# Kernel tuning notes

Hardware: AMD Instinct MI355X
Metric: run time of the kernel (lower is better)

## Reference

```python
import jax, jax.numpy as jnp
import numpy as np

N, E, D_IN, D_H, D_OUT = 8000, 256000, 128, 128, 64
TEMP = 10.0       # config temperature.value (non-learnable)
WEIGHT = 1.0      # config weight.value (non-learnable)
LN_EPS = 1e-5


def _gcn_conv(x, W, b, src, dst, n):
    # PyG GCNConv: add self loops, sym-normalized aggregation, then bias.
    h = x @ W
    loop = jnp.arange(n)
    s = jnp.concatenate([src, loop])
    d = jnp.concatenate([dst, loop])
    deg = jnp.zeros((n,), h.dtype).at[d].add(1.0)
    dinv = jax.lax.rsqrt(jnp.maximum(deg, 1e-12))
    norm = dinv[s] * dinv[d]                       # [E+N]
    out = jax.ops.segment_sum(h[s] * norm[:, None], d, num_segments=n)
    return out + b


def _entropy_gradient(x, A, temperature, normalize):
    # E_i = 0.5 * sum_j A_ij ||x_i - x_j||^2  (dense adjacency, as in repo)
    sq = jnp.sum(x * x, axis=1)                    # [N]
    Ax = A @ x                                     # [N,d]
    deg = A.sum(axis=1)                            # [N]
    En = 0.5 * (deg * sq + A @ sq - 2.0 * jnp.sum(x * Ax, axis=1))
    if normalize:
        En = En / (jnp.max(En) + 1e-12)
    logits = -En / temperature
    P = jax.nn.softmax(logits)
    logP = jax.nn.log_softmax(logits)
    S = -jnp.sum(P * logP)
    c = P * (logP + S) / temperature               # dS/dE_k
    # dS/dx_i = c_i*(deg_i x_i - (Ax)_i) + (A^T c)_i x_i - (A^T (c*x))_i
    ATc = A.T @ c
    return (c[:, None] * (deg[:, None] * x - Ax)
            + ATc[:, None] * x - A.T @ (c[:, None] * x))


def _layer_norm(x, gamma, beta):
    mu = jnp.mean(x, axis=-1, keepdims=True)
    var = jnp.mean(jnp.square(x - mu), axis=-1, keepdims=True)
    return (x - mu) * jax.lax.rsqrt(var + LN_EPS) * gamma + beta


def setup_inputs() -> dict:
    key = jax.random.key(0)
    ks = jax.random.split(key, 6)
    def w(k, i, o):
        return jax.random.normal(k, (i, o), jnp.float32) / np.sqrt(i).astype(np.float32)
    return {
        "x": jax.random.normal(ks[0], (N, D_IN), jnp.float32),
        "edge_index": jax.random.randint(ks[1], (2, E), 0, N),
        "W1": w(ks[2], D_IN, D_H), "b1": jnp.zeros((D_H,), jnp.float32),
        "W2": w(ks[3], D_H, D_H), "b2": jnp.zeros((D_H,), jnp.float32),
        "W_out": w(ks[4], D_H, D_OUT), "b_out": jnp.zeros((D_OUT,), jnp.float32),
        "ln_gamma": jnp.ones((D_H,), jnp.float32),
        "ln_beta": jnp.zeros((D_H,), jnp.float32),
    }


def reference(x, edge_index, W1, b1, W2, b2, W_out, b_out, ln_gamma, ln_beta):
    n = x.shape[0]
    src, dst = edge_index[0], edge_index[1]
    # dense adjacency (to_dense_adj sums duplicate edges)
    A = jnp.zeros((n, n), x.dtype).at[src, dst].add(1.0)
    for W, b in ((W1, b1), (W2, b2)):
        h = _gcn_conv(x, W, b, src, dst, n)
        eg = jax.lax.stop_gradient(_entropy_gradient(h, A, TEMP, True))
        h = h + WEIGHT * eg
        h = jax.nn.relu(h)
        x = _layer_norm(h, ln_gamma, ln_beta)
    embedding = _gcn_conv(x, W_out, b_out, src, dst, n)
    return embedding
```

## Files before the change

### kernel.cpp

```cpp
#include <hip/hip_runtime.h>
#include <hip/hip_bf16.h>

#define DH 128
#define NCOPY 8

static constexpr float TEMP_ = 10.0f;
static constexpr float LN_EPS_ = 1e-5f;

__device__ __forceinline__ unsigned short f2bf(float f) {
  union { float f; unsigned int i; } v; v.f = f;
  unsigned int b = v.i + 0x7FFFu + ((v.i >> 16) & 1u);
  return (unsigned short)(b >> 16);
}
__device__ __forceinline__ void dec2(unsigned int u, float& lo, float& hi) {
  union { unsigned int i; float f; } a, b;
  a.i = u << 16; b.i = u & 0xFFFF0000u;
  lo = a.f; hi = b.f;
}
__device__ __forceinline__ void dec8(uint4 u, float* o) {
  dec2(u.x, o[0], o[1]); dec2(u.y, o[2], o[3]);
  dec2(u.z, o[4], o[5]); dec2(u.w, o[6], o[7]);
}
__device__ __forceinline__ unsigned int pack2(float lo, float hi) {
  return (unsigned int)f2bf(lo) | ((unsigned int)f2bf(hi) << 16);
}

__device__ __forceinline__ float grp_sum16(float v) {
  #pragma unroll
  for (int o = 8; o > 0; o >>= 1) v += __shfl_down(v, o, 16);
  return __shfl(v, 0, 16);
}

__device__ __forceinline__ float blkred(float v, bool mx, float* s4) {
  const int t = threadIdx.x;
  #pragma unroll
  for (int o = 32; o > 0; o >>= 1) {
    float u = __shfl_down(v, o, 64);
    v = mx ? fmaxf(v, u) : v + u;
  }
  __syncthreads();
  if ((t & 63) == 0) s4[t >> 6] = v;
  __syncthreads();
  float r = mx ? fmaxf(fmaxf(s4[0], s4[1]), fmaxf(s4[2], s4[3]))
               : (s4[0] + s4[1]) + (s4[2] + s4[3]);
  __syncthreads();
  return r;
}

__global__ __launch_bounds__(256) void k_gemm1_hist(const float* __restrict__ X,
                                                    const float* __restrict__ W,
                                                    unsigned short* __restrict__ Hb,
                                                    const int* __restrict__ ei, int E,
                                                    int* cnt_d, int* cnt_s,
                                                    int NT, int N) {
  __shared__ float Ws[64 * DH];
  __shared__ float xs[16 * 128];
  const int t = threadIdx.x;
  if ((int)blockIdx.x < NT) {
    const int row0 = blockIdx.x * 16;
    const float4* xg = (const float4*)(X + row0 * 128);
    float4* xs4 = (float4*)xs;
    xs4[t] = xg[t];
    xs4[t + 256] = xg[t + 256];
    const int c = t & 127, rg = t >> 7;
    float acc[8];
    #pragma unroll
    for (int r = 0; r < 8; ++r) acc[r] = 0.f;
    for (int kt = 0; kt < 2; ++kt) {
      __syncthreads();
      for (int i = t; i < 64 * DH; i += 256) Ws[i] = W[kt * 64 * DH + i];
      __syncthreads();
      for (int k = 0; k < 64; ++k) {
        float wv = Ws[k * DH + c];
        #pragma unroll
        for (int r = 0; r < 8; ++r)
          acc[r] += xs[(rg * 8 + r) * 128 + kt * 64 + k] * wv;
      }
    }
    #pragma unroll
    for (int r = 0; r < 8; ++r)
      Hb[(row0 + rg * 8 + r) * DH + c] = f2bf(acc[r]);
  } else {
    const int nb = gridDim.x - NT;
    for (int e = (blockIdx.x - NT) * 256 + t; e < E; e += nb * 256) {
      int cp = (e >> 5) & (NCOPY - 1);
      atomicAdd(&cnt_s[cp * N + ei[e]], 1);
      atomicAdd(&cnt_d[cp * N + ei[E + e]], 1);
    }
  }
}

template <int DOUT>
__global__ __launch_bounds__(256) void k_gemm(const float* __restrict__ X,
                                              const float* __restrict__ W,
                                              unsigned short* __restrict__ Hb) {
  __shared__ float Ws[64 * DOUT];
  __shared__ float xs[16 * 128];
  const int t = threadIdx.x;
  const int row0 = blockIdx.x * 16;

  const float4* xg = (const float4*)(X + row0 * 128);
  float4* xs4 = (float4*)xs;
  xs4[t] = xg[t];
  xs4[t + 256] = xg[t + 256];

  constexpr int RPT = (16 * DOUT) / 256;
  const int c = t % DOUT;
  const int rg = t / DOUT;
  float acc[RPT];
  #pragma unroll
  for (int r = 0; r < RPT; ++r) acc[r] = 0.f;

  for (int kt = 0; kt < 2; ++kt) {
    __syncthreads();
    for (int i = t; i < 64 * DOUT; i += 256) Ws[i] = W[kt * 64 * DOUT + i];
    __syncthreads();
    for (int k = 0; k < 64; ++k) {
      float wv = Ws[k * DOUT + c];
      #pragma unroll
      for (int r = 0; r < RPT; ++r)
        acc[r] += xs[(rg * RPT + r) * 128 + kt * 64 + k] * wv;
    }
  }
  #pragma unroll
  for (int r = 0; r < RPT; ++r)
    Hb[(row0 + rg * RPT + r) * DOUT + c] = f2bf(acc[r]);
}

__global__ __launch_bounds__(256) void k_scan_a(int* cnt_d, int* cnt_s,
                                                int* off_d, int* off_s,
                                                int* bsum,
                                                float* dinv, float* dego, int n) {
  __shared__ int ws4[4];
  const int t = threadIdx.x;
  const int dir = blockIdx.x >> 5, blk = blockIdx.x & 31;
  int* cnt = dir ? cnt_s : cnt_d;
  int* off = dir ? off_s : off_d;
  const int NPB = (n + 31) >> 5;
  const int i = blk * NPB + t;
  const bool valid = (t < NPB) && (i < n);
  int tot = 0;
  if (valid) {
    #pragma unroll
    for (int c = 0; c < NCOPY; ++c) tot += cnt[c * n + i];
  }
  const int lane = t & 63, w = t >> 6;
  int v = tot;
  #pragma unroll
  for (int o = 1; o < 64; o <<= 1) {
    int u = __shfl_up(v, o, 64);
    if (lane >= o) v += u;
  }
  if (lane == 63) ws4[w] = v;
  __syncthreads();
  int wbase = 0;
  #pragma unroll
  for (int k = 0; k < 4; ++k) wbase += (k < w) ? ws4[k] : 0;
  const int excl = wbase + v - tot;
  if (valid) {
    off[i] = excl;
    if (dir == 0) dinv[i] = rsqrtf((float)tot + 1.0f);
    else          dego[i] = (float)tot;
  }
  if (t == 0) {
    int bt = 0;
    #pragma unroll
    for (int k = 0; k < 4; ++k) bt += ws4[k];
    bsum[dir * 32 + blk] = bt;
  }
}

__global__ __launch_bounds__(256) void k_scan_b(int* cnt_d, int* cnt_s,
                                                int* off_d, int* off_s,
                                                int* base_d, int* base_s,
                                                const int* __restrict__ bsum, int n) {
  __shared__ int sb;
  const int t = threadIdx.x;
  const int dir = blockIdx.x >> 5, blk = blockIdx.x & 31;
  int* cnt  = dir ? cnt_s  : cnt_d;
  int* off  = dir ? off_s  : off_d;
  int* base = dir ? base_s : base_d;
  if (t == 0) {
    int s = 0;
    for (int k = 0; k < blk; ++k) s += bsum[dir * 32 + k];
    sb = s;
  }
  __syncthreads();
  const int bbase = sb;
  const int NPB = (n + 31) >> 5;
  const int i = blk * NPB + t;
  if (t < NPB && i < n) {
    int o = bbase + off[i];
    off[i] = o;
    int rc = o;
    #pragma unroll
    for (int c = 0; c < NCOPY; ++c) {
      base[c * n + i] = rc;
      rc += cnt[c * n + i];
      cnt[c * n + i] = 0;
    }
  }
  if (t == 1 && blk == 31) {
    int s = 0;
    for (int k = 0; k < 32; ++k) s += bsum[dir * 32 + k];
    off[n] = s;
  }
}

__global__ void k_fill(const int* __restrict__ ei, int E,
                       const int* __restrict__ base_d, const int* __restrict__ base_s,
                       int* cnt_d, int* cnt_s, int* idx_d, int* idx_s, int N) {
  int e = blockIdx.x * blockDim.x + threadIdx.x;
  if (e < E) {
    int cp = (e >> 5) & (NCOPY - 1);
    int s = ei[e], d = ei[E + e];
    int p = atomicAdd(&cnt_d[cp * N + d], 1);
    idx_d[base_d[cp * N + d] + p] = s;
    int q = atomicAdd(&cnt_s[cp * N + s], 1);
    idx_s[base_s[cp * N + s] + q] = d;
  }
}

__global__ __launch_bounds__(256) void k_conv_agg(const unsigned short* __restrict__ Hb,
                                                  const float* __restrict__ dinv,
                                                  const float* __restrict__ b,
                                                  const int* __restrict__ off_d,
                                                  const int* __restrict__ idx_d,
                                                  float* __restrict__ G,
                                                  unsigned short* __restrict__ Gb,
                                                  float* __restrict__ sq) {
  const int lane = threadIdx.x & 15;
  const int i = blockIdx.x * 16 + (threadIdx.x >> 4);
  const uint4* Hv = (const uint4*)Hb;
  const float di = dinv[i];
  float acc[8];
  {
    float t8[8]; dec8(Hv[i * 16 + lane], t8);
    #pragma unroll
    for (int k = 0; k < 8; ++k) acc[k] = di * t8[k];
  }
  int o = off_d[i];
  const int oe = off_d[i + 1];
  for (; o + 8 <= oe; o += 8) {
    int s[8]; float dv[8]; uint4 r[8];
    #pragma unroll
    for (int j = 0; j < 8; ++j) s[j] = idx_d[o + j];
    #pragma unroll
    for (int j = 0; j < 8; ++j) { r[j] = Hv[s[j] * 16 + lane]; dv[j] = dinv[s[j]]; }
    #pragma unroll
    for (int j = 0; j < 8; ++j) {
      float t8[8]; dec8(r[j], t8);
      #pragma unroll
      for (int k = 0; k < 8; ++k) acc[k] = fmaf(dv[j], t8[k], acc[k]);
    }
  }
  for (; o < oe; ++o) {
    int s = idx_d[o];
    float dvs = dinv[s];
    float t8[8]; dec8(Hv[s * 16 + lane], t8);
    #pragma unroll
    for (int k = 0; k < 8; ++k) acc[k] = fmaf(dvs, t8[k], acc[k]);
  }
  const float4 b0 = ((const float4*)b)[lane * 2];
  const float4 b1 = ((const float4*)b)[lane * 2 + 1];
  float gi[8];
  gi[0] = fmaf(di, acc[0], b0.x); gi[1] = fmaf(di, acc[1], b0.y);
  gi[2] = fmaf(di, acc[2], b0.z); gi[3] = fmaf(di, acc[3], b0.w);
  gi[4] = fmaf(di, acc[4], b1.x); gi[5] = fmaf(di, acc[5], b1.y);
  gi[6] = fmaf(di, acc[6], b1.z); gi[7] = fmaf(di, acc[7], b1.w);
  ((float4*)G)[i * 32 + lane * 2]     = make_float4(gi[0], gi[1], gi[2], gi[3]);
  ((float4*)G)[i * 32 + lane * 2 + 1] = make_float4(gi[4], gi[5], gi[6], gi[7]);
  uint4 gp;
  gp.x = pack2(gi[0], gi[1]); gp.y = pack2(gi[2], gi[3]);
  gp.z = pack2(gi[4], gi[5]); gp.w = pack2(gi[6], gi[7]);
  ((uint4*)Gb)[i * 16 + lane] = gp;
  float s2 = 0.f;
  #pragma unroll
  for (int k = 0; k < 8; ++k) s2 += gi[k] * gi[k];
  s2 = grp_sum16(s2);
  if (lane == 0) sq[i] = s2;
}

__global__ __launch_bounds__(256) void k_ax_en(const float* __restrict__ G,
                                               const unsigned short* __restrict__ Gb,
                                               const float* __restrict__ sq,
                                               const float* __restrict__ dego,
                                               const int* __restrict__ off_s,
                                               const int* __restrict__ idx_s,
                                               float* __restrict__ Ax,
                                               float* __restrict__ En) {
  const int lane = threadIdx.x & 15;
  const int i = blockIdx.x * 16 + (threadIdx.x >> 4);
  const uint4* Gv = (const uint4*)Gb;
  float axf[8];
  #pragma unroll
  for (int k = 0; k < 8; ++k) axf[k] = 0.f;
  float asq = 0.f;
  int o = off_s[i];
  const int oe = off_s[i + 1];
  for (; o + 8 <= oe; o += 8) {
    int s[8]; float qv[8]; uint4 r[8];
    #pragma unroll
    for (int j = 0; j < 8; ++j) s[j] = idx_s[o + j];
    #pragma unroll
    for (int j = 0; j < 8; ++j) { r[j] = Gv[s[j] * 16 + lane]; qv[j] = sq[s[j]]; }
    #pragma unroll
    for (int j = 0; j < 8; ++j) {
      float t8[8]; dec8(r[j], t8);
      asq += qv[j];
      #pragma unroll
      for (int k = 0; k < 8; ++k) axf[k] += t8[k];
    }
  }
  for (; o < oe; ++o) {
    int s = idx_s[o];
    float t8[8]; dec8(Gv[s * 16 + lane], t8);
    asq += sq[s];
    #pragma unroll
    for (int k = 0; k < 8; ++k) axf[k] += t8[k];
  }
  ((float4*)Ax)[i * 32 + lane * 2]     = make_float4(axf[0], axf[1], axf[2], axf[3]);
  ((float4*)Ax)[i * 32 + lane * 2 + 1] = make_float4(axf[4], axf[5], axf[6], axf[7]);
  const float4 g0 = ((const float4*)G)[i * 32 + lane * 2];
  const float4 g1 = ((const float4*)G)[i * 32 + lane * 2 + 1];
  float dot = g0.x * axf[0] + g0.y * axf[1] + g0.z * axf[2] + g0.w * axf[3]
            + g1.x * axf[4] + g1.y * axf[5] + g1.z * axf[6] + g1.w * axf[7];
  dot = grp_sum16(dot);
  if (lane == 0) En[i] = 0.5f * (dego[i] * sq[i] + asq - 2.f * dot);
}

__global__ __launch_bounds__(256) void k_combine_ln(const float* __restrict__ G,
                                                    const unsigned short* __restrict__ Gb,
                                                    const float* __restrict__ Ax,
                                                    const float* __restrict__ En,
                                                    const float* __restrict__ dego,
                                                    const int* __restrict__ off_d,
                                                    const int* __restrict__ idx_d,
                                                    const float* __restrict__ gamma,
                                                    const float* __restrict__ beta,
                                                    float* __restrict__ Xout, int n) {
  __shared__ float s4[4];
  const int t = threadIdx.x;
  float mloc = -3.0e38f;
  for (int k = t; k < n; k += 256) mloc = fmaxf(mloc, En[k]);
  const float m = blkred(mloc, true, s4);
  const float invden = -1.0f / ((m + 1e-12f) * TEMP_);
  float se = 0.f, sl = 0.f;
  for (int k = t; k < n; k += 256) {
    float li = En[k] * invden;
    float e = __expf(li);
    se += e; sl += e * li;
  }
  se = blkred(se, false, s4);
  sl = blkred(sl, false, s4);
  const float logZ = __logf(se);
  const float S = logZ - sl / se;
  const float cmul = (1.0f / se) * (1.0f / TEMP_);
  const float cadd = S - logZ;

  const int lane = t & 15;
  const int i = blockIdx.x * 16 + (t >> 4);
  const uint4* Gv = (const uint4*)Gb;
  const float4 g0 = ((const float4*)G)[i * 32 + lane * 2];
  const float4 g1 = ((const float4*)G)[i * 32 + lane * 2 + 1];
  const float gi[8] = { g0.x, g0.y, g0.z, g0.w, g1.x, g1.y, g1.z, g1.w };
  float tf[8];
  #pragma unroll
  for (int k = 0; k < 8; ++k) tf[k] = 0.f;
  float atc = 0.f;
  int o = off_d[i];
  const int oe = off_d[i + 1];
  for (; o + 8 <= oe; o += 8) {
    int s[8]; float ev[8]; uint4 r[8];
    #pragma unroll
    for (int j = 0; j < 8; ++j) s[j] = idx_d[o + j];
    #pragma unroll
    for (int j = 0; j < 8; ++j) { r[j] = Gv[s[j] * 16 + lane]; ev[j] = En[s[j]]; }
    #pragma unroll
    for (int j = 0; j < 8; ++j) {
      float ls = ev[j] * invden;
      float cs = __expf(ls) * cmul * (ls + cadd);
      atc += cs;
      float t8[8]; dec8(r[j], t8);
      #pragma unroll
      for (int k = 0; k < 8; ++k) tf[k] = fmaf(cs, t8[k], tf[k]);
    }
  }
  for (; o < oe; ++o) {
    int s = idx_d[o];
    float ls = En[s] * invden;
    float cs = __expf(ls) * cmul * (ls + cadd);
    atc += cs;
    float t8[8]; dec8(Gv[s * 16 + lane], t8);
    #pragma unroll
    for (int k = 0; k < 8; ++k) tf[k] = fmaf(cs, t8[k], tf[k]);
  }
  const float li_i = En[i] * invden;
  const float ci = __expf(li_i) * cmul * (li_i + cadd);
  const float dg = dego[i];
  const float4 a0 = ((const float4*)Ax)[i * 32 + lane * 2];
  const float4 a1 = ((const float4*)Ax)[i * 32 + lane * 2 + 1];
  const float axi[8] = { a0.x, a0.y, a0.z, a0.w, a1.x, a1.y, a1.z, a1.w };
  float v[8];
  float ssum = 0.f;
  #pragma unroll
  for (int k = 0; k < 8; ++k) {
    v[k] = fmaxf(gi[k] + ci * (dg * gi[k] - axi[k]) + atc * gi[k] - tf[k], 0.f);
    ssum += v[k];
  }
  float mu = grp_sum16(ssum) * (1.f / 128.f);
  float vsum = 0.f;
  #pragma unroll
  for (int k = 0; k < 8; ++k) {
    v[k] -= mu;
    vsum += v[k] * v[k];
  }
  float var = grp_sum16(vsum) * (1.f / 128.f);
  float rs = rsqrtf(var + LN_EPS_);
  const float4 ga0 = ((const float4*)gamma)[lane * 2];
  const float4 ga1 = ((const float4*)gamma)[lane * 2 + 1];
  const float4 be0 = ((const float4*)beta)[lane * 2];
  const float4 be1 = ((const float4*)beta)[lane * 2 + 1];
  float4 o0, o1;
  o0.x = fmaf(v[0] * rs, ga0.x, be0.x); o0.y = fmaf(v[1] * rs, ga0.y, be0.y);
  o0.z = fmaf(v[2] * rs, ga0.z, be0.z); o0.w = fmaf(v[3] * rs, ga0.w, be0.w);
  o1.x = fmaf(v[4] * rs, ga1.x, be1.x); o1.y = fmaf(v[5] * rs, ga1.y, be1.y);
  o1.z = fmaf(v[6] * rs, ga1.z, be1.z); o1.w = fmaf(v[7] * rs, ga1.w, be1.w);
  ((float4*)Xout)[i * 32 + lane * 2]     = o0;
  ((float4*)Xout)[i * 32 + lane * 2 + 1] = o1;
}

__global__ __launch_bounds__(256) void k_final_agg(const unsigned short* __restrict__ Hb,
                                                   const float* __restrict__ dinv,
                                                   const float* __restrict__ bout,
                                                   const int* __restrict__ off_d,
                                                   const int* __restrict__ idx_d,
                                                   float* __restrict__ out) {
  const int lane = threadIdx.x & 7;
  const int i = blockIdx.x * 32 + (threadIdx.x >> 3);
  const uint4* Hv = (const uint4*)Hb;
  const float di = dinv[i];
  float acc[8];
  {
    float t8[8]; dec8(Hv[i * 8 + lane], t8);
    #pragma unroll
    for (int k = 0; k < 8; ++k) acc[k] = di * t8[k];
  }
  int o = off_d[i];
  const int oe = off_d[i + 1];
  for (; o + 8 <= oe; o += 8) {
    int s[8]; float dv[8]; uint4 r[8];
    #pragma unroll
    for (int j = 0; j < 8; ++j) s[j] = idx_d[o + j];
    #pragma unroll
    for (int j = 0; j < 8; ++j) { r[j] = Hv[s[j] * 8 + lane]; dv[j] = dinv[s[j]]; }
    #pragma unroll
    for (int j = 0; j < 8; ++j) {
      float t8[8]; dec8(r[j], t8);
      #pragma unroll
      for (int k = 0; k < 8; ++k) acc[k] = fmaf(dv[j], t8[k], acc[k]);
    }
  }
  for (; o < oe; ++o) {
    int s = idx_d[o];
    float dvs = dinv[s];
    float t8[8]; dec8(Hv[s * 8 + lane], t8);
    #pragma unroll
    for (int k = 0; k < 8; ++k) acc[k] = fmaf(dvs, t8[k], acc[k]);
  }
  const float4 b0 = ((const float4*)bout)[lane * 2];
  const float4 b1 = ((const float4*)bout)[lane * 2 + 1];
  float4 r0, r1;
  r0.x = fmaf(di, acc[0], b0.x); r0.y = fmaf(di, acc[1], b0.y);
  r0.z = fmaf(di, acc[2], b0.z); r0.w = fmaf(di, acc[3], b0.w);
  r1.x = fmaf(di, acc[4], b1.x); r1.y = fmaf(di, acc[5], b1.y);
  r1.z = fmaf(di, acc[6], b1.z); r1.w = fmaf(di, acc[7], b1.w);
  ((float4*)out)[i * 16 + lane * 2]     = r0;
  ((float4*)out)[i * 16 + lane * 2 + 1] = r1;
}

extern "C" void kernel_launch(void* const* d_in, const int* in_sizes, int n_in,
                              void* d_out, int out_size, void* d_ws, size_t ws_size,
                              hipStream_t stream) {
  const float* x    = (const float*)d_in[0];
  const int*   ei   = (const int*)d_in[1];
  const float* W1   = (const float*)d_in[2];
  const float* b1   = (const float*)d_in[3];
  const float* W2   = (const float*)d_in[4];
  const float* b2   = (const float*)d_in[5];
  const float* Wout = (const float*)d_in[6];
  const float* bout = (const float*)d_in[7];
  const float* gam  = (const float*)d_in[8];
  const float* bet  = (const float*)d_in[9];
  float* out = (float*)d_out;

  const int N = in_sizes[0] / DH;
  const int E = in_sizes[1] / 2;

  float* ws = (float*)d_ws;
  float* xf = ws;   ws += N * DH;
  float* G  = ws;   ws += N * DH;
  float* Ax = ws;   ws += N * DH;
  float* sq = ws;   ws += N;
  float* En = ws;   ws += N;
  float* dinv = ws; ws += N;
  float* dego = ws; ws += N;
  unsigned short* Hb = (unsigned short*)ws; ws += N * DH / 2;
  unsigned short* Gb = (unsigned short*)ws; ws += N * DH / 2;
  int* cnt_d  = (int*)ws; ws += NCOPY * N;
  int* cnt_s  = (int*)ws; ws += NCOPY * N;
  int* base_d = (int*)ws; ws += NCOPY * N;
  int* base_s = (int*)ws; ws += NCOPY * N;
  int* off_d  = (int*)ws; ws += N + 4;
  int* off_s  = (int*)ws; ws += N + 4;
  int* bsum   = (int*)ws; ws += 64;
  int* idx_d  = (int*)ws; ws += E;
  int* idx_s  = (int*)ws; ws += E;

  const int NT = N / 16;

  hipMemsetAsync(cnt_d, 0, 2 * NCOPY * N * sizeof(int), stream);
  k_gemm1_hist<<<NT + 256, 256, 0, stream>>>(x, W1, Hb, ei, E, cnt_d, cnt_s, NT, N);
  k_scan_a<<<64, 256, 0, stream>>>(cnt_d, cnt_s, off_d, off_s, bsum, dinv, dego, N);
  k_scan_b<<<64, 256, 0, stream>>>(cnt_d, cnt_s, off_d, off_s, base_d, base_s,
                                   bsum, N);
  k_fill<<<(E + 255) / 256, 256, 0, stream>>>(ei, E, base_d, base_s,
                                              cnt_d, cnt_s, idx_d, idx_s, N);

  for (int l = 0; l < 2; ++l) {
    if (l) k_gemm<DH><<<N / 16, 256, 0, stream>>>(xf, W2, Hb);
    k_conv_agg<<<N / 16, 256, 0, stream>>>(Hb, dinv, l ? b2 : b1, off_d, idx_d,
                                           G, Gb, sq);
    k_ax_en<<<N / 16, 256, 0, stream>>>(G, Gb, sq, dego, off_s, idx_s, Ax, En);
    k_combine_ln<<<N / 16, 256, 0, stream>>>(G, Gb, Ax, En, dego, off_d, idx_d,
                                             gam, bet, xf, N);
  }
  k_gemm<64><<<N / 16, 256, 0, stream>>>(xf, Wout, Hb);
  k_final_agg<<<N / 32, 256, 0, stream>>>(Hb, dinv, bout, off_d, idx_d, out);
}
```

Measured before the change: 249.2 us.

## Fuse LayerNorm with next GEMM and drop replicated histogram counters

Merges the combine+LayerNorm kernel with the following dense GEMM, so each block writes its normalized 16-row tile to shared memory and multiplies it by W2 or W_out directly. This removes the fp32 xf round trip through global memory and two kernel launches. Separately, the 8-way replicated degree counters used for the CSR histogram and fill are collapsed to a single copy, which simplifies the scans and drops the base arrays. That risks more atomic contention on hot nodes during the histogram and fill.

```diff
diff --git a/kernel.cpp b/kernel.cpp
--- a/kernel.cpp
+++ b/kernel.cpp
@@ -2,7 +2,6 @@
 #include <hip/hip_bf16.h>
 
 #define DH 128
-#define NCOPY 8
 
 static constexpr float TEMP_ = 10.0f;
 static constexpr float LN_EPS_ = 1e-5f;
@@ -51,8 +50,7 @@
                                                     const float* __restrict__ W,
                                                     unsigned short* __restrict__ Hb,
                                                     const int* __restrict__ ei, int E,
-                                                    int* cnt_d, int* cnt_s,
-                                                    int NT, int N) {
+                                                    int* cnt_d, int* cnt_s, int NT) {
   __shared__ float Ws[64 * DH];
   __shared__ float xs[16 * 128];
   const int t = threadIdx.x;
@@ -83,67 +81,25 @@
   } else {
     const int nb = gridDim.x - NT;
     for (int e = (blockIdx.x - NT) * 256 + t; e < E; e += nb * 256) {
-      int cp = (e >> 5) & (NCOPY - 1);
-      atomicAdd(&cnt_s[cp * N + ei[e]], 1);
-      atomicAdd(&cnt_d[cp * N + ei[E + e]], 1);
-    }
-  }
-}
-
-template <int DOUT>
-__global__ __launch_bounds__(256) void k_gemm(const float* __restrict__ X,
-                                              const float* __restrict__ W,
-                                              unsigned short* __restrict__ Hb) {
-  __shared__ float Ws[64 * DOUT];
-  __shared__ float xs[16 * 128];
-  const int t = threadIdx.x;
-  const int row0 = blockIdx.x * 16;
-
-  const float4* xg = (const float4*)(X + row0 * 128);
-  float4* xs4 = (float4*)xs;
-  xs4[t] = xg[t];
-  xs4[t + 256] = xg[t + 256];
-
-  constexpr int RPT = (16 * DOUT) / 256;
-  const int c = t % DOUT;
-  const int rg = t / DOUT;
-  float acc[RPT];
-  #pragma unroll
-  for (int r = 0; r < RPT; ++r) acc[r] = 0.f;
-
-  for (int kt = 0; kt < 2; ++kt) {
-    __syncthreads();
-    for (int i = t; i < 64 * DOUT; i += 256) Ws[i] = W[kt * 64 * DOUT + i];
-    __syncthreads();
-    for (int k = 0; k < 64; ++k) {
-      float wv = Ws[k * DOUT + c];
-      #pragma unroll
-      for (int r = 0; r < RPT; ++r)
-        acc[r] += xs[(rg * RPT + r) * 128 + kt * 64 + k] * wv;
-    }
-  }
-  #pragma unroll
-  for (int r = 0; r < RPT; ++r)
-    Hb[(row0 + rg * RPT + r) * DOUT + c] = f2bf(acc[r]);
-}
-
-__global__ __launch_bounds__(256) void k_scan_a(int* cnt_d, int* cnt_s,
-                                                int* off_d, int* off_s,
-                                                int* bsum,
+      atomicAdd(&cnt_s[ei[e]], 1);
+      atomicAdd(&cnt_d[ei[E + e]], 1);
+    }
+  }
+}
+
+__global__ __launch_bounds__(256) void k_scan_a(const int* __restrict__ cnt_d,
+                                                const int* __restrict__ cnt_s,
+                                                int* off_d, int* off_s, int* bsum,
                                                 float* dinv, float* dego, int n) {
   __shared__ int ws4[4];
   const int t = threadIdx.x;
   const int dir = blockIdx.x >> 5, blk = blockIdx.x & 31;
-  int* cnt = dir ? cnt_s : cnt_d;
+  const int* cnt = dir ? cnt_s : cnt_d;
   int* off = dir ? off_s : off_d;
   const int NPB = (n + 31) >> 5;
   const int i = blk * NPB + t;
   const bool valid = (t < NPB) && (i < n);
-  int tot = 0;
-  if (valid) {
-    #pragma unroll
-    for (int c = 0; c < NCOPY; ++c) tot += cnt[c * n + i];
-  }
+  int tot = valid ? cnt[i] : 0;
   const int lane = t & 63, w = t >> 6;
   int v = tot;
   #pragma unroll
@@ -172,14 +128,12 @@
 
 __global__ __launch_bounds__(256) void k_scan_b(int* cnt_d, int* cnt_s,
                                                 int* off_d, int* off_s,
-                                                int* base_d, int* base_s,
                                                 const int* __restrict__ bsum, int n) {
   __shared__ int sb;
   const int t = threadIdx.x;
   const int dir = blockIdx.x >> 5, blk = blockIdx.x & 31;
-  int* cnt  = dir ? cnt_s  : cnt_d;
-  int* off  = dir ? off_s  : off_d;
-  int* base = dir ? base_s : base_d;
+  int* cnt = dir ? cnt_s : cnt_d;
+  int* off = dir ? off_s : off_d;
   if (t == 0) {
     int s = 0;
     for (int k = 0; k < blk; ++k) s += bsum[dir * 32 + k];
@@ -190,15 +144,8 @@
   const int NPB = (n + 31) >> 5;
   const int i = blk * NPB + t;
   if (t < NPB && i < n) {
-    int o = bbase + off[i];
-    off[i] = o;
-    int rc = o;
-    #pragma unroll
-    for (int c = 0; c < NCOPY; ++c) {
-      base[c * n + i] = rc;
-      rc += cnt[c * n + i];
-      cnt[c * n + i] = 0;
-    }
+    off[i] = bbase + off[i];
+    cnt[i] = 0;
   }
   if (t == 1 && blk == 31) {
     int s = 0;
@@ -208,16 +155,15 @@
 }
 
 __global__ void k_fill(const int* __restrict__ ei, int E,
-                       const int* __restrict__ base_d, const int* __restrict__ base_s,
-                       int* cnt_d, int* cnt_s, int* idx_d, int* idx_s, int N) {
+                       const int* __restrict__ off_d, const int* __restrict__ off_s,
+                       int* cnt_d, int* cnt_s, int* idx_d, int* idx_s) {
   int e = blockIdx.x * blockDim.x + threadIdx.x;
   if (e < E) {
-    int cp = (e >> 5) & (NCOPY - 1);
     int s = ei[e], d = ei[E + e];
-    int p = atomicAdd(&cnt_d[cp * N + d], 1);
-    idx_d[base_d[cp * N + d] + p] = s;
-    int q = atomicAdd(&cnt_s[cp * N + s], 1);
-    idx_s[base_s[cp * N + s] + q] = d;
+    int p = atomicAdd(&cnt_d[d], 1);
+    idx_d[off_d[d] + p] = s;
+    int q = atomicAdd(&cnt_s[s], 1);
+    idx_s[off_s[s] + q] = d;
   }
 }
 
@@ -329,16 +275,21 @@
   if (lane == 0) En[i] = 0.5f * (dego[i] * sq[i] + asq - 2.f * dot);
 }
 
-__global__ __launch_bounds__(256) void k_combine_ln(const float* __restrict__ G,
-                                                    const unsigned short* __restrict__ Gb,
-                                                    const float* __restrict__ Ax,
-                                                    const float* __restrict__ En,
-                                                    const float* __restrict__ dego,
-                                                    const int* __restrict__ off_d,
-                                                    const int* __restrict__ idx_d,
-                                                    const float* __restrict__ gamma,
-                                                    const float* __restrict__ beta,
-                                                    float* __restrict__ Xout, int n) {
+template <int DOUT>
+__global__ __launch_bounds__(256) void k_combine_gemm(const float* __restrict__ G,
+                                                      const unsigned short* __restrict__ Gb,
+                                                      const float* __restrict__ Ax,
+                                                      const float* __restrict__ En,
+                                                      const float* __restrict__ dego,
+                                                      const int* __restrict__ off_d,
+                                                      const int* __restrict__ idx_d,
+                                                      const float* __restrict__ gamma,
+                                                      const float* __restrict__ beta,
+                                                      const float* __restrict__ W,
+                                                      unsigned short* __restrict__ Hb,
+                                                      int n) {
+  __shared__ float Ws[64 * DOUT];
+  __shared__ float xs[16 * 128];
   __shared__ float s4[4];
   const int t = threadIdx.x;
   float mloc = -3.0e38f;
@@ -426,8 +377,32 @@
   o0.z = fmaf(v[2] * rs, ga0.z, be0.z); o0.w = fmaf(v[3] * rs, ga0.w, be0.w);
   o1.x = fmaf(v[4] * rs, ga1.x, be1.x); o1.y = fmaf(v[5] * rs, ga1.y, be1.y);
   o1.z = fmaf(v[6] * rs, ga1.z, be1.z); o1.w = fmaf(v[7] * rs, ga1.w, be1.w);
-  ((float4*)Xout)[i * 32 + lane * 2]     = o0;
-  ((float4*)Xout)[i * 32 + lane * 2 + 1] = o1;
+
+  float* xrow = xs + (t >> 4) * 128 + lane * 8;
+  ((float4*)xrow)[0] = o0;
+  ((float4*)xrow)[1] = o1;
+
+  const int row0 = blockIdx.x * 16;
+  constexpr int RPT = (16 * DOUT) / 256;
+  const int c = t % DOUT;
+  const int rg = t / DOUT;
+  float acc[RPT];
+  #pragma unroll
+  for (int r = 0; r < RPT; ++r) acc[r] = 0.f;
+  for (int kt = 0; kt < 2; ++kt) {
+    if (kt) __syncthreads();
+    for (int idx = t; idx < 64 * DOUT; idx += 256) Ws[idx] = W[kt * 64 * DOUT + idx];
+    __syncthreads();
+    for (int k = 0; k < 64; ++k) {
+      float wv = Ws[k * DOUT + c];
+      #pragma unroll
+      for (int r = 0; r < RPT; ++r)
+        acc[r] += xs[(rg * RPT + r) * 128 + kt * 64 + k] * wv;
+    }
+  }
+  #pragma unroll
+  for (int r = 0; r < RPT; ++r)
+    Hb[(row0 + rg * RPT + r) * DOUT + c] = f2bf(acc[r]);
 }
 
 __global__ __launch_bounds__(256) void k_final_agg(const unsigned short* __restrict__ Hb,
@@ -498,7 +473,6 @@
   const int E = in_sizes[1] / 2;
 
   float* ws = (float*)d_ws;
-  float* xf = ws;   ws += N * DH;
   float* G  = ws;   ws += N * DH;
   float* Ax = ws;   ws += N * DH;
   float* sq = ws;   ws += N;
@@ -507,10 +481,8 @@
   float* dego = ws; ws += N;
   unsigned short* Hb = (unsigned short*)ws; ws += N * DH / 2;
   unsigned short* Gb = (unsigned short*)ws; ws += N * DH / 2;
-  int* cnt_d  = (int*)ws; ws += NCOPY * N;
-  int* cnt_s  = (int*)ws; ws += NCOPY * N;
-  int* base_d = (int*)ws; ws += NCOPY * N;
-  int* base_s = (int*)ws; ws += NCOPY * N;
+  int* cnt_d  = (int*)ws; ws += N;
+  int* cnt_s  = (int*)ws; ws += N;
   int* off_d  = (int*)ws; ws += N + 4;
   int* off_s  = (int*)ws; ws += N + 4;
   int* bsum   = (int*)ws; ws += 64;
@@ -519,22 +491,20 @@
 
   const int NT = N / 16;
 
-  hipMemsetAsync(cnt_d, 0, 2 * NCOPY * N * sizeof(int), stream);
-  k_gemm1_hist<<<NT + 256, 256, 0, stream>>>(x, W1, Hb, ei, E, cnt_d, cnt_s, NT, N);
+  hipMemsetAsync(cnt_d, 0, 2 * N * sizeof(int), stream);
+  k_gemm1_hist<<<NT + 256, 256, 0, stream>>>(x, W1, Hb, ei, E, cnt_d, cnt_s, NT);
   k_scan_a<<<64, 256, 0, stream>>>(cnt_d, cnt_s, off_d, off_s, bsum, dinv, dego, N);
-  k_scan_b<<<64, 256, 0, stream>>>(cnt_d, cnt_s, off_d, off_s, base_d, base_s,
-                                   bsum, N);
-  k_fill<<<(E + 255) / 256, 256, 0, stream>>>(ei, E, base_d, base_s,
-                                              cnt_d, cnt_s, idx_d, idx_s, N);
-
-  for (int l = 0; l < 2; ++l) {
-    if (l) k_gemm<DH><<<N / 16, 256, 0, stream>>>(xf, W2, Hb);
-    k_conv_agg<<<N / 16, 256, 0, stream>>>(Hb, dinv, l ? b2 : b1, off_d, idx_d,
-                                           G, Gb, sq);
-    k_ax_en<<<N / 16, 256, 0, stream>>>(G, Gb, sq, dego, off_s, idx_s, Ax, En);
-    k_combine_ln<<<N / 16, 256, 0, stream>>>(G, Gb, Ax, En, dego, off_d, idx_d,
-                                             gam, bet, xf, N);
-  }
-  k_gemm<64><<<N / 16, 256, 0, stream>>>(xf, Wout, Hb);
+  k_scan_b<<<64, 256, 0, stream>>>(cnt_d, cnt_s, off_d, off_s, bsum, N);
+  k_fill<<<(E + 255) / 256, 256, 0, stream>>>(ei, E, off_d, off_s, cnt_d, cnt_s,
+                                              idx_d, idx_s);
+
+  k_conv_agg<<<N / 16, 256, 0, stream>>>(Hb, dinv, b1, off_d, idx_d, G, Gb, sq);
+  k_ax_en<<<N / 16, 256, 0, stream>>>(G, Gb, sq, dego, off_s, idx_s, Ax, En);
+  k_combine_gemm<128><<<N / 16, 256, 0, stream>>>(G, Gb, Ax, En, dego, off_d,
+                                                  idx_d, gam, bet, W2, Hb, N);
+  k_conv_agg<<<N / 16, 256, 0, stream>>>(Hb, dinv, b2, off_d, idx_d, G, Gb, sq);
+  k_ax_en<<<N / 16, 256, 0, stream>>>(G, Gb, sq, dego, off_s, idx_s, Ax, En);
+  k_combine_gemm<64><<<N / 16, 256, 0, stream>>>(G, Gb, Ax, En, dego, off_d,
+                                                 idx_d, gam, bet, Wout, Hb, N);
   k_final_agg<<<N / 32, 256, 0, stream>>>(Hb, dinv, bout, off_d, idx_d, out);
 }
```

After: 237.9 us. 4.5% less time.
